# Performance work log

Measured on AMD Instinct MI355X. Metric: run time of the kernel, lower is better.

## Reference

```python
import jax, jax.numpy as jnp
import numpy as np

B, N, M = 16, 2048, 2048


def setup_inputs() -> dict:
    key = jax.random.key(0)
    k1, k2, k3 = jax.random.split(key, 3)
    pred_dsmat = jax.random.uniform(k1, (B, N, M), dtype=jnp.float32)
    # valid sizes: src_ns <= tgt_ns so a permutation GT exists for every valid row
    src_ns = jax.random.randint(k2, (B,), 1024, 1537, dtype=jnp.int32)
    tgt_ns = jax.random.randint(k3, (B,), 1537, 2049, dtype=jnp.int32)
    # gt_perm: identity permutation restricted to the valid region (one 1 per valid row)
    i = jnp.arange(N)[:, None]
    j = jnp.arange(M)[None, :]
    eye = (i == j).astype(jnp.float32)  # [N, M]
    row_mask = (jnp.arange(N)[None, :] < src_ns[:, None]).astype(jnp.float32)  # [B, N]
    gt_perm = eye[None, :, :] * row_mask[:, :, None]  # [B, N, M]
    return {"pred_dsmat": pred_dsmat, "gt_perm": gt_perm,
            "src_ns": src_ns, "tgt_ns": tgt_ns, "beta_value": 0.1}


def reference(pred_dsmat, gt_perm, src_ns, tgt_ns, beta_value):
    Bn, Nn, Mn = pred_dsmat.shape
    row_mask = jnp.arange(Nn)[None, :] < src_ns[:, None]   # [B, N] bool
    col_mask = jnp.arange(Mn)[None, :] < tgt_ns[:, None]   # [B, M] bool
    mask = row_mask[:, :, None] & col_mask[:, None, :]     # [B, N, M]

    pred = jnp.clip(pred_dsmat, 0.0, 1.0) * mask
    gt = gt_perm * mask

    gt_pred = pred * gt                      # gt-selected predicted values
    row_gt = gt_pred.sum(axis=2)             # [B, N] per-row GT value
    col_gt = gt_pred.sum(axis=1)             # [B, M] per-col GT value
    row_cnt = gt.sum(axis=2)                 # [B, N] #GT matches per row
    col_cnt = gt.sum(axis=1)                 # [B, M] #GT matches per col

    # attention masks: entries >= (gt value - beta), restricted to valid region
    att_src = ((pred >= row_gt[:, :, None] - beta_value) & mask) * row_cnt[:, :, None]
    att_tgt = ((pred >= col_gt[:, None, :] - beta_value) & mask) * col_cnt[:, None, :]

    src_neg = jnp.sum(((att_src - gt) * pred) ** 2, axis=2)  # [B, N]
    src_pos = jnp.sum(gt_pred ** 2, axis=2)                  # [B, N]
    tgt_neg = jnp.sum(((att_tgt - gt) * pred) ** 2, axis=1)  # [B, M]

    # sum of tgt_neg over the GT-matched column of each row == dot with column counts
    corr = jnp.einsum('bm,bm->b', tgt_neg, col_cnt)          # [B]

    denom = 1.0 + src_neg + corr[:, None]                    # [B, N]
    num = jnp.where(row_mask, src_pos, 1.0)
    den = jnp.where(row_mask, denom, 1.0)
    loss = -0.5 * jnp.sum(jnp.log(num / den) * row_mask)
    n_sum = src_ns.sum().astype(pred.dtype)
    return loss / n_sum
```

## Files before the change

kernel.cpp:

```cpp
#include <hip/hip_runtime.h>

#define B_ 16
#define N_ 2048
#define M_ 2048
#define RROWS 16
#define WROWS 4
#define CHUNK 1024
#define NCHUNK (M_ / CHUNK)
#define JCH (CHUNK / 256)
#define DROWS 32
#define DWROWS 8
#define KCAP 4

__device__ __forceinline__ float wave_sum(float v) {
#pragma unroll
    for (int off = 32; off >= 1; off >>= 1) v += __shfl_xor(v, off);
    return v;
}

extern "C" __global__ __launch_bounds__(256) void k_gt(
    const float* __restrict__ gt,
    const int* __restrict__ src_ns, const int* __restrict__ tgt_ns,
    int* __restrict__ nnz, int* __restrict__ ent_col,
    float* __restrict__ ent_val, int* flag)
{
    const int b = blockIdx.y;
    const int src = src_ns[b];
    const int band = blockIdx.x;
    if (band * RROWS >= src) return;
    const int tgt = tgt_ns[b];
    const int c0 = blockIdx.z * CHUNK;
    if (tgt - c0 <= 0) return;
    const int wave = threadIdx.x >> 6, lane = threadIdx.x & 63;
    const int bc = b * (N_ * M_) + c0;

    const int row0 = band * RROWS + wave * WROWS;
    for (int r = 0; r < WROWS; ++r) {
        const int n = row0 + r;
        if (n >= src) break;
        const int ri = b * N_ + n;
        const float4* grow = (const float4*)(gt + bc + n * M_);
        const float4 g0 = grow[lane];
        const float4 g1 = grow[64 + lane];
        const float4 g2 = grow[128 + lane];
        const float4 g3 = grow[192 + lane];
#define GTEST(GV, J) \
        if (GV.x != 0.f || GV.y != 0.f || GV.z != 0.f || GV.w != 0.f) { \
            const int mb = c0 + (J * 64 + lane) * 4; \
            GC(GV, 0, x); GC(GV, 1, y); GC(GV, 2, z); GC(GV, 3, w); \
        }
#define GC(GV, KK, MB) do { \
    const int c = mb + KK; \
    const float gv = GV.MB; \
    if (gv != 0.f && c < tgt) { \
        const int slot = atomicAdd(&nnz[ri], 1); \
        if (slot < KCAP) { ent_col[ri * KCAP + slot] = c; ent_val[ri * KCAP + slot] = gv; } \
        else *flag = 1; \
    } \
} while (0)
        GTEST(g0, 0) GTEST(g1, 1) GTEST(g2, 2) GTEST(g3, 3)
#undef GC
#undef GTEST
    }
}

extern "C" __global__ __launch_bounds__(256) void k_mid(
    const float* __restrict__ pred,
    const int* __restrict__ src_ns,
    const int* __restrict__ nnz, const int* __restrict__ ent_col,
    const float* __restrict__ ent_val, const int* flag,
    float* __restrict__ row_gt, float* __restrict__ row_cnt,
    float* __restrict__ col_gt, float* __restrict__ col_cnt)
{
    if (*flag) return;
    const int ri = blockIdx.x * 256 + threadIdx.x;
    const int b = ri >> 11, n = ri & (N_ - 1);
    if (n >= src_ns[b]) { row_gt[ri] = 0.f; row_cnt[ri] = 0.f; return; }
    const int nn0 = nnz[ri];
    const int nn = nn0 < KCAP ? nn0 : KCAP;
    float rg = 0.f, rc = 0.f;
    for (int s = 0; s < nn; ++s) {
        const int c = ent_col[ri * KCAP + s];
        const float gv = ent_val[ri * KCAP + s];
        float p = pred[b * (N_ * M_) + n * M_ + c];
        p = fminf(fmaxf(p, 0.f), 1.f);
        rg += gv * p; rc += gv;
        atomicAdd(&col_gt[b * M_ + c], gv * p);
        atomicAdd(&col_cnt[b * M_ + c], gv);
    }
    row_gt[ri] = rg; row_cnt[ri] = rc;
}

extern "C" __global__ __launch_bounds__(256) void k_p1d(
    const float* __restrict__ pred, const float* __restrict__ gt,
    const int* __restrict__ src_ns, const int* __restrict__ tgt_ns,
    const int* flag,
    float* __restrict__ row_gt, float* __restrict__ row_cnt,
    float* __restrict__ col_gt, float* __restrict__ col_cnt)
{
    if (*flag == 0) return;
    const int b = blockIdx.y;
    const int src = src_ns[b];
    const int band = blockIdx.x;
    if (band * DROWS >= src) return;
    const int tgt = tgt_ns[b];
    const int wave = threadIdx.x >> 6, lane = threadIdx.x & 63;
    const int base = b * (N_ * M_);

    float4 acg[8], accn[8];
#pragma unroll
    for (int j = 0; j < 8; ++j) { acg[j] = make_float4(0,0,0,0); accn[j] = make_float4(0,0,0,0); }

    const int row0 = band * DROWS + wave * DWROWS;
    for (int r = 0; r < DWROWS; ++r) {
        const int n = row0 + r;
        if (n >= src) break;
        const float4* prow = (const float4*)(pred + base + n * M_);
        const float4* grow = (const float4*)(gt + base + n * M_);
        float rg = 0.f, rc = 0.f;
#pragma unroll
        for (int j = 0; j < 8; ++j) {
            const int m4 = j * 64 + lane;
            const float4 p4 = prow[m4];
            const float4 g4 = grow[m4];
            const int mb = m4 * 4;
#define P1C(KK, MB) do { \
    const bool ok = (mb + KK) < tgt; \
    float p = fminf(fmaxf(p4.MB, 0.f), 1.f); p = ok ? p : 0.f; \
    const float g = ok ? g4.MB : 0.f; \
    const float gp = p * g; \
    rg += gp; rc += g; \
    acg[j].MB += gp; accn[j].MB += g; \
} while (0)
            P1C(0, x); P1C(1, y); P1C(2, z); P1C(3, w);
#undef P1C
        }
        rg = wave_sum(rg); rc = wave_sum(rc);
        if (lane == 0) { row_gt[b * N_ + n] = rg; row_cnt[b * N_ + n] = rc; }
    }

    __shared__ float4 s_cg[M_ / 4];
    __shared__ float4 s_cc[M_ / 4];
    for (int i = threadIdx.x; i < M_ / 4; i += 256) {
        s_cg[i] = make_float4(0,0,0,0);
        s_cc[i] = make_float4(0,0,0,0);
    }
    __syncthreads();
    for (int w = 0; w < 4; ++w) {
        if (wave == w) {
#pragma unroll
            for (int j = 0; j < 8; ++j) {
                const int i = j * 64 + lane;
                float4 v = s_cg[i];
                v.x += acg[j].x; v.y += acg[j].y; v.z += acg[j].z; v.w += acg[j].w;
                s_cg[i] = v;
                float4 u = s_cc[i];
                u.x += accn[j].x; u.y += accn[j].y; u.z += accn[j].z; u.w += accn[j].w;
                s_cc[i] = u;
            }
        }
        __syncthreads();
    }
    const float* fcg = (const float*)s_cg;
    const float* fcc = (const float*)s_cc;
    for (int i = threadIdx.x; i < M_; i += 256) {
        atomicAdd(&col_gt[b * M_ + i], fcg[i]);
        atomicAdd(&col_cnt[b * M_ + i], fcc[i]);
    }
}

extern "C" __global__ __launch_bounds__(256) void k_pred(
    const float* __restrict__ pred, const float* __restrict__ gt,
    const int* __restrict__ src_ns, const int* __restrict__ tgt_ns,
    const float* __restrict__ beta_p,
    const float* __restrict__ row_gt, const float* __restrict__ row_cnt,
    const float* __restrict__ col_gt, const float* __restrict__ col_cnt,
    const int* __restrict__ nnz, const int* __restrict__ ent_col,
    const float* __restrict__ ent_val, const int* flag,
    float* __restrict__ src_neg, float* __restrict__ src_pos,
    float* __restrict__ corr)
{
    const int b = blockIdx.y;
    const int src = src_ns[b];
    const int band = blockIdx.x;
    if (band * RROWS >= src) return;
    const int tgt = tgt_ns[b];
    const int c0 = blockIdx.z * CHUNK;
    const bool chunk0 = (c0 == 0);
    if (tgt - c0 <= 0 && !chunk0) return;
    const float beta = beta_p[0];
    const int wave = threadIdx.x >> 6, lane = threadIdx.x & 63;
    const int bfull = b * (N_ * M_);
    const int bc = bfull + c0;
    const bool dense = (*flag != 0);

    float4 cgb[JCH], cc[JCH], tn[JCH];
    const float4* cg4 = (const float4*)(col_gt + b * M_ + c0);
    const float4* cc4 = (const float4*)(col_cnt + b * M_ + c0);
#pragma unroll
    for (int j = 0; j < JCH; ++j) {
        float4 v = cg4[j * 64 + lane];
        v.x -= beta; v.y -= beta; v.z -= beta; v.w -= beta;
        cgb[j] = v;
        cc[j] = cc4[j * 64 + lane];
        tn[j] = make_float4(0,0,0,0);
    }

    float cadd = 0.f;
    const int row0 = band * RROWS + wave * WROWS;
    if (!dense) {
        for (int r = 0; r < WROWS; ++r) {
            const int n = row0 + r;
            if (n >= src) break;
            const int ri = b * N_ + n;
            const float rc = row_cnt[ri];
            const float rth = row_gt[ri] - beta;
            const float4* prow = (const float4*)(pred + bc + n * M_);
            const float4 p0 = prow[lane];
            const float4 p1 = prow[64 + lane];
            const float4 p2 = prow[128 + lane];
            const float4 p3 = prow[192 + lane];
            float sneg = 0.f;
#define P2S(PV, J, KK, MB) do { \
    const bool ok = (c0 + (J * 64 + lane) * 4 + KK) < tgt; \
    float p = fminf(fmaxf(PV.MB, 0.f), 1.f); p = ok ? p : 0.f; \
    const float as = (p >= rth) ? rc : 0.f; \
    const float ds = as * p; \
    sneg += ds * ds; \
    const float at = (p >= cgb[J].MB) ? cc[J].MB : 0.f; \
    const float d = at * p; \
    tn[J].MB += d * d; \
} while (0)
#define P2SV(PV, J) P2S(PV, J, 0, x); P2S(PV, J, 1, y); P2S(PV, J, 2, z); P2S(PV, J, 3, w);
            P2SV(p0, 0) P2SV(p1, 1) P2SV(p2, 2) P2SV(p3, 3)
#undef P2SV
#undef P2S
            sneg = wave_sum(sneg);
            if (lane == 0) {
                if (chunk0) {
                    float spos = 0.f;
                    const int nn0 = nnz[ri];
                    const int nn = nn0 < KCAP ? nn0 : KCAP;
                    for (int s = 0; s < nn; ++s) {
                        const int c = ent_col[ri * KCAP + s];
                        const float gv = ent_val[ri * KCAP + s];
                        float pv = pred[bfull + n * M_ + c];
                        pv = fminf(fmaxf(pv, 0.f), 1.f);
                        const float as = (pv >= rth) ? rc : 0.f;
                        const float d0 = as * pv;
                        const float d1 = (as - gv) * pv;
                        sneg += d1 * d1 - d0 * d0;
                        const float gp = gv * pv;
                        spos += gp * gp;
                        const float ccv = col_cnt[b * M_ + c];
                        const float at = (pv >= col_gt[b * M_ + c] - beta) ? ccv : 0.f;
                        const float t0 = at * pv;
                        const float t1 = (at - gv) * pv;
                        cadd += (t1 * t1 - t0 * t0) * ccv;
                    }
                    atomicAdd(&src_pos[ri], spos);
                }
                atomicAdd(&src_neg[ri], sneg);
            }
        }
    } else {
        for (int r = 0; r < WROWS; ++r) {
            const int n = row0 + r;
            if (n >= src) break;
            const int ri = b * N_ + n;
            const float rc = row_cnt[ri];
            const float rth = row_gt[ri] - beta;
            const float4* prow = (const float4*)(pred + bc + n * M_);
            const float4* grow = (const float4*)(gt + bc + n * M_);
            const float4 p0 = prow[lane];
            const float4 p1 = prow[64 + lane];
            const float4 p2 = prow[128 + lane];
            const float4 p3 = prow[192 + lane];
            const float4 g0 = grow[lane];
            const float4 g1 = grow[64 + lane];
            const float4 g2 = grow[128 + lane];
            const float4 g3 = grow[192 + lane];
            float sneg = 0.f, spos = 0.f;
#define P2D(PV, GV, J, KK, MB) do { \
    const bool ok = (c0 + (J * 64 + lane) * 4 + KK) < tgt; \
    float p = fminf(fmaxf(PV.MB, 0.f), 1.f); p = ok ? p : 0.f; \
    const float gv = ok ? GV.MB : 0.f; \
    const float as = (p >= rth) ? rc : 0.f; \
    const float ds = (as - gv) * p; \
    sneg += ds * ds; \
    const float gp = gv * p; spos += gp * gp; \
    const float at = (p >= cgb[J].MB) ? cc[J].MB : 0.f; \
    const float dt = (at - gv) * p; \
    tn[J].MB += dt * dt; \
} while (0)
#define P2DV(PV, GV, J) P2D(PV, GV, J, 0, x); P2D(PV, GV, J, 1, y); P2D(PV, GV, J, 2, z); P2D(PV, GV, J, 3, w);
            P2DV(p0, g0, 0) P2DV(p1, g1, 1) P2DV(p2, g2, 2) P2DV(p3, g3, 3)
#undef P2DV
#undef P2D
            sneg = wave_sum(sneg); spos = wave_sum(spos);
            if (lane == 0) {
                atomicAdd(&src_neg[ri], sneg);
                atomicAdd(&src_pos[ri], spos);
            }
        }
    }

    float dp = cadd;
#pragma unroll
    for (int j = 0; j < JCH; ++j)
        dp += tn[j].x * cc[j].x + tn[j].y * cc[j].y + tn[j].z * cc[j].z + tn[j].w * cc[j].w;
    dp = wave_sum(dp);
    __shared__ float sred[4];
    if (lane == 0) sred[wave] = dp;
    __syncthreads();
    if (threadIdx.x == 0)
        atomicAdd(&corr[b], sred[0] + sred[1] + sred[2] + sred[3]);
}

extern "C" __global__ __launch_bounds__(256) void k_final(
    const float* __restrict__ src_neg, const float* __restrict__ src_pos,
    const float* __restrict__ corr_p, const int* __restrict__ src_ns,
    float* __restrict__ out)
{
    const int b = blockIdx.x >> 2;
    const int part = blockIdx.x & 3;
    const int wave = threadIdx.x >> 6, lane = threadIdx.x & 63;
    const int src = src_ns[b];
    const int n0 = part * (N_ / 4);
    const int n1 = n0 + (N_ / 4);
    const float corr = corr_p[b];

    float ls = 0.f;
    for (int n = n0 + threadIdx.x; n < n1 && n < src; n += 256) {
        const float sp = src_pos[b * N_ + n];
        const float sn = src_neg[b * N_ + n];
        ls += logf(sp) - logf(1.f + sn + corr);
    }
    ls = wave_sum(ls);
    __shared__ float sredl[4];
    if (lane == 0) sredl[wave] = ls;
    __syncthreads();
    if (threadIdx.x == 0) {
        const float total = sredl[0] + sredl[1] + sredl[2] + sredl[3];
        float nsum = 0.f;
        for (int i = 0; i < B_; ++i) nsum += (float)src_ns[i];
        atomicAdd(out, -0.5f * total / nsum);
    }
}

extern "C" void kernel_launch(void* const* d_in, const int* in_sizes, int n_in,
                              void* d_out, int out_size, void* d_ws, size_t ws_size,
                              hipStream_t stream)
{
    const float* pred   = (const float*)d_in[0];
    const float* gtp    = (const float*)d_in[1];
    const int*   src_ns = (const int*)d_in[2];
    const int*   tgt_ns = (const int*)d_in[3];
    const float* beta   = (const float*)d_in[4];
    float* out = (float*)d_out;
    float* ws  = (float*)d_ws;

    float* col_gt  = ws;
    float* col_cnt = col_gt  + B_ * M_;
    float* src_neg = col_cnt + B_ * M_;
    float* src_pos = src_neg + B_ * N_;
    float* corr    = src_pos + B_ * N_;
    int*   nnz     = (int*)(corr + B_);
    int*   flag    = nnz + B_ * N_;
    float* row_gt  = (float*)(flag + 1);
    float* row_cnt = row_gt + B_ * N_;
    int*   ent_col = (int*)(row_cnt + B_ * N_);
    float* ent_val = (float*)(ent_col + B_ * N_ * KCAP);

    const size_t zero_bytes = (size_t)(2 * B_ * M_ + 3 * B_ * N_ + B_ + 1) * sizeof(float);
    hipMemsetAsync(d_ws, 0, zero_bytes, stream);
    hipMemsetAsync(d_out, 0, sizeof(float), stream);

    dim3 gsplit(N_ / RROWS, B_, NCHUNK);
    k_gt<<<gsplit, 256, 0, stream>>>(gtp, src_ns, tgt_ns, nnz, ent_col, ent_val, flag);
    k_mid<<<(B_ * N_) / 256, 256, 0, stream>>>(pred, src_ns, nnz, ent_col, ent_val, flag,
                                               row_gt, row_cnt, col_gt, col_cnt);
    k_p1d<<<dim3(N_ / DROWS, B_), 256, 0, stream>>>(pred, gtp, src_ns, tgt_ns, flag,
                                                    row_gt, row_cnt, col_gt, col_cnt);
    k_pred<<<gsplit, 256, 0, stream>>>(pred, gtp, src_ns, tgt_ns, beta,
                                       row_gt, row_cnt, col_gt, col_cnt,
                                       nnz, ent_col, ent_val, flag,
                                       src_neg, src_pos, corr);
    k_final<<<B_ * 4, 256, 0, stream>>>(src_neg, src_pos, corr, src_ns, out);
}
```

Baseline: 500.0 us.

## Fuse row/col GT accumulation into k_gt, drop k_mid, shrink row bands

Folds the per-row and per-column GT value/count accumulation into the sparse GT scan kernel using atomics, removing the separate k_mid launch. Because the dense fallback can no longer share the column buffers, separate sparse and dense column arrays are kept and selected in k_pred. Rows per block are halved for k_gt and k_pred to raise block count, and k_final uses more blocks with one row per thread. The cost is more atomics in the scan kernel, a larger workspace memset, and possible partial sparse accumulations if the overflow flag trips mid-scan.

```diff
diff --git a/kernel.cpp b/kernel.cpp
--- a/kernel.cpp
+++ b/kernel.cpp
@@ -3,8 +3,8 @@
 #define B_ 16
 #define N_ 2048
 #define M_ 2048
-#define RROWS 16
-#define WROWS 4
+#define RROWS 8
+#define WROWS 2
 #define CHUNK 1024
 #define NCHUNK (M_ / CHUNK)
 #define JCH (CHUNK / 256)
@@ -19,10 +19,13 @@
 }
 
 extern "C" __global__ __launch_bounds__(256) void k_gt(
-    const float* __restrict__ gt,
+    const float* __restrict__ gt, const float* __restrict__ pred,
     const int* __restrict__ src_ns, const int* __restrict__ tgt_ns,
     int* __restrict__ nnz, int* __restrict__ ent_col,
-    float* __restrict__ ent_val, int* flag)
+    float* __restrict__ ent_val,
+    float* __restrict__ row_gt, float* __restrict__ row_cnt,
+    float* __restrict__ colS_gt, float* __restrict__ colS_cnt,
+    int* flag)
 {
     const int b = blockIdx.y;
     const int src = src_ns[b];
@@ -32,7 +35,8 @@
     const int c0 = blockIdx.z * CHUNK;
     if (tgt - c0 <= 0) return;
     const int wave = threadIdx.x >> 6, lane = threadIdx.x & 63;
-    const int bc = b * (N_ * M_) + c0;
+    const int bfull = b * (N_ * M_);
+    const int bc = bfull + c0;
 
     const int row0 = band * RROWS + wave * WROWS;
     for (int r = 0; r < WROWS; ++r) {
@@ -54,8 +58,16 @@
     const float gv = GV.MB; \
     if (gv != 0.f && c < tgt) { \
         const int slot = atomicAdd(&nnz[ri], 1); \
-        if (slot < KCAP) { ent_col[ri * KCAP + slot] = c; ent_val[ri * KCAP + slot] = gv; } \
-        else *flag = 1; \
+        if (slot < KCAP) { \
+            ent_col[ri * KCAP + slot] = c; ent_val[ri * KCAP + slot] = gv; \
+            float pv = pred[bfull + n * M_ + c]; \
+            pv = fminf(fmaxf(pv, 0.f), 1.f); \
+            const float gp = gv * pv; \
+            atomicAdd(&row_gt[ri], gp); \
+            atomicAdd(&row_cnt[ri], gv); \
+            atomicAdd(&colS_gt[b * M_ + c], gp); \
+            atomicAdd(&colS_cnt[b * M_ + c], gv); \
+        } else *flag = 1; \
     } \
 } while (0)
         GTEST(g0, 0) GTEST(g1, 1) GTEST(g2, 2) GTEST(g3, 3)
@@ -64,39 +76,12 @@
     }
 }
 
-extern "C" __global__ __launch_bounds__(256) void k_mid(
-    const float* __restrict__ pred,
-    const int* __restrict__ src_ns,
-    const int* __restrict__ nnz, const int* __restrict__ ent_col,
-    const float* __restrict__ ent_val, const int* flag,
-    float* __restrict__ row_gt, float* __restrict__ row_cnt,
-    float* __restrict__ col_gt, float* __restrict__ col_cnt)
-{
-    if (*flag) return;
-    const int ri = blockIdx.x * 256 + threadIdx.x;
-    const int b = ri >> 11, n = ri & (N_ - 1);
-    if (n >= src_ns[b]) { row_gt[ri] = 0.f; row_cnt[ri] = 0.f; return; }
-    const int nn0 = nnz[ri];
-    const int nn = nn0 < KCAP ? nn0 : KCAP;
-    float rg = 0.f, rc = 0.f;
-    for (int s = 0; s < nn; ++s) {
-        const int c = ent_col[ri * KCAP + s];
-        const float gv = ent_val[ri * KCAP + s];
-        float p = pred[b * (N_ * M_) + n * M_ + c];
-        p = fminf(fmaxf(p, 0.f), 1.f);
-        rg += gv * p; rc += gv;
-        atomicAdd(&col_gt[b * M_ + c], gv * p);
-        atomicAdd(&col_cnt[b * M_ + c], gv);
-    }
-    row_gt[ri] = rg; row_cnt[ri] = rc;
-}
-
 extern "C" __global__ __launch_bounds__(256) void k_p1d(
     const float* __restrict__ pred, const float* __restrict__ gt,
     const int* __restrict__ src_ns, const int* __restrict__ tgt_ns,
     const int* flag,
     float* __restrict__ row_gt, float* __restrict__ row_cnt,
-    float* __restrict__ col_gt, float* __restrict__ col_cnt)
+    float* __restrict__ colD_gt, float* __restrict__ colD_cnt)
 {
     if (*flag == 0) return;
     const int b = blockIdx.y;
@@ -164,8 +149,8 @@
     const float* fcg = (const float*)s_cg;
     const float* fcc = (const float*)s_cc;
     for (int i = threadIdx.x; i < M_; i += 256) {
-        atomicAdd(&col_gt[b * M_ + i], fcg[i]);
-        atomicAdd(&col_cnt[b * M_ + i], fcc[i]);
+        atomicAdd(&colD_gt[b * M_ + i], fcg[i]);
+        atomicAdd(&colD_cnt[b * M_ + i], fcc[i]);
     }
 }
 
@@ -174,7 +159,8 @@
     const int* __restrict__ src_ns, const int* __restrict__ tgt_ns,
     const float* __restrict__ beta_p,
     const float* __restrict__ row_gt, const float* __restrict__ row_cnt,
-    const float* __restrict__ col_gt, const float* __restrict__ col_cnt,
+    const float* __restrict__ colS_gt, const float* __restrict__ colS_cnt,
+    const float* __restrict__ colD_gt, const float* __restrict__ colD_cnt,
     const int* __restrict__ nnz, const int* __restrict__ ent_col,
     const float* __restrict__ ent_val, const int* flag,
     float* __restrict__ src_neg, float* __restrict__ src_pos,
@@ -193,10 +179,12 @@
     const int bfull = b * (N_ * M_);
     const int bc = bfull + c0;
     const bool dense = (*flag != 0);
+    const float* __restrict__ cgq = dense ? colD_gt : colS_gt;
+    const float* __restrict__ ccq = dense ? colD_cnt : colS_cnt;
 
     float4 cgb[JCH], cc[JCH], tn[JCH];
-    const float4* cg4 = (const float4*)(col_gt + b * M_ + c0);
-    const float4* cc4 = (const float4*)(col_cnt + b * M_ + c0);
+    const float4* cg4 = (const float4*)(cgq + b * M_ + c0);
+    const float4* cc4 = (const float4*)(ccq + b * M_ + c0);
 #pragma unroll
     for (int j = 0; j < JCH; ++j) {
         float4 v = cg4[j * 64 + lane];
@@ -252,8 +240,8 @@
                         sneg += d1 * d1 - d0 * d0;
                         const float gp = gv * pv;
                         spos += gp * gp;
-                        const float ccv = col_cnt[b * M_ + c];
-                        const float at = (pv >= col_gt[b * M_ + c] - beta) ? ccv : 0.f;
+                        const float ccv = ccq[b * M_ + c];
+                        const float at = (pv >= cgq[b * M_ + c] - beta) ? ccv : 0.f;
                         const float t0 = at * pv;
                         const float t1 = (at - gv) * pv;
                         cadd += (t1 * t1 - t0 * t0) * ccv;
@@ -322,19 +310,19 @@
     const float* __restrict__ corr_p, const int* __restrict__ src_ns,
     float* __restrict__ out)
 {
-    const int b = blockIdx.x >> 2;
-    const int part = blockIdx.x & 3;
+    const int b = blockIdx.x >> 3;
+    const int part = blockIdx.x & 7;
     const int wave = threadIdx.x >> 6, lane = threadIdx.x & 63;
     const int src = src_ns[b];
-    const int n0 = part * (N_ / 4);
-    const int n1 = n0 + (N_ / 4);
+    const int n0 = part * (N_ / 8);
     const float corr = corr_p[b];
 
     float ls = 0.f;
-    for (int n = n0 + threadIdx.x; n < n1 && n < src; n += 256) {
+    const int n = n0 + threadIdx.x;
+    if (n < src) {
         const float sp = src_pos[b * N_ + n];
         const float sn = src_neg[b * N_ + n];
-        ls += logf(sp) - logf(1.f + sn + corr);
+        ls = logf(sp) - logf(1.f + sn + corr);
     }
     ls = wave_sum(ls);
     __shared__ float sredl[4];
@@ -342,9 +330,11 @@
     __syncthreads();
     if (threadIdx.x == 0) {
         const float total = sredl[0] + sredl[1] + sredl[2] + sredl[3];
-        float nsum = 0.f;
-        for (int i = 0; i < B_; ++i) nsum += (float)src_ns[i];
-        atomicAdd(out, -0.5f * total / nsum);
+        if (total != 0.f) {
+            float nsum = 0.f;
+            for (int i = 0; i < B_; ++i) nsum += (float)src_ns[i];
+            atomicAdd(out, -0.5f * total / nsum);
+        }
     }
 }
 
@@ -360,31 +350,34 @@
     float* out = (float*)d_out;
     float* ws  = (float*)d_ws;
 
-    float* col_gt  = ws;
-    float* col_cnt = col_gt  + B_ * M_;
-    float* src_neg = col_cnt + B_ * M_;
-    float* src_pos = src_neg + B_ * N_;
-    float* corr    = src_pos + B_ * N_;
-    int*   nnz     = (int*)(corr + B_);
-    int*   flag    = nnz + B_ * N_;
-    float* row_gt  = (float*)(flag + 1);
-    float* row_cnt = row_gt + B_ * N_;
-    int*   ent_col = (int*)(row_cnt + B_ * N_);
-    float* ent_val = (float*)(ent_col + B_ * N_ * KCAP);
-
-    const size_t zero_bytes = (size_t)(2 * B_ * M_ + 3 * B_ * N_ + B_ + 1) * sizeof(float);
+    float* colS_gt  = ws;
+    float* colS_cnt = colS_gt  + B_ * M_;
+    float* colD_gt  = colS_cnt + B_ * M_;
+    float* colD_cnt = colD_gt  + B_ * M_;
+    float* row_gt   = colD_cnt + B_ * M_;
+    float* row_cnt  = row_gt   + B_ * N_;
+    float* src_neg  = row_cnt  + B_ * N_;
+    float* src_pos  = src_neg  + B_ * N_;
+    float* corr     = src_pos  + B_ * N_;
+    int*   nnz      = (int*)(corr + B_);
+    int*   flag     = nnz + B_ * N_;
+    int*   ent_col  = (int*)(flag + 1);
+    float* ent_val  = (float*)(ent_col + B_ * N_ * KCAP);
+
+    const size_t zero_bytes = (size_t)(4 * B_ * M_ + 5 * B_ * N_ + B_ + 1) * sizeof(float);
     hipMemsetAsync(d_ws, 0, zero_bytes, stream);
     hipMemsetAsync(d_out, 0, sizeof(float), stream);
 
     dim3 gsplit(N_ / RROWS, B_, NCHUNK);
-    k_gt<<<gsplit, 256, 0, stream>>>(gtp, src_ns, tgt_ns, nnz, ent_col, ent_val, flag);
-    k_mid<<<(B_ * N_) / 256, 256, 0, stream>>>(pred, src_ns, nnz, ent_col, ent_val, flag,
-                                               row_gt, row_cnt, col_gt, col_cnt);
+    k_gt<<<gsplit, 256, 0, stream>>>(gtp, pred, src_ns, tgt_ns,
+                                     nnz, ent_col, ent_val,
+                                     row_gt, row_cnt, colS_gt, colS_cnt, flag);
     k_p1d<<<dim3(N_ / DROWS, B_), 256, 0, stream>>>(pred, gtp, src_ns, tgt_ns, flag,
-                                                    row_gt, row_cnt, col_gt, col_cnt);
+                                                    row_gt, row_cnt, colD_gt, colD_cnt);
     k_pred<<<gsplit, 256, 0, stream>>>(pred, gtp, src_ns, tgt_ns, beta,
-                                       row_gt, row_cnt, col_gt, col_cnt,
+                                       row_gt, row_cnt,
+                                       colS_gt, colS_cnt, colD_gt, colD_cnt,
                                        nnz, ent_col, ent_val, flag,
                                        src_neg, src_pos, corr);
-    k_final<<<B_ * 4, 256, 0, stream>>>(src_neg, src_pos, corr, src_ns, out);
-}
+    k_final<<<B_ * 8, 256, 0, stream>>>(src_neg, src_pos, corr, src_ns, out);
+}
```

Result: slower. 515.9 us (+3.2%).
